# Kernel optimization log

Measured on AMD Instinct MI355X. Metric: run time of the kernel, lower is better.

## Reference

```python
import jax, jax.numpy as jnp
import numpy as np

N0, N1, N2 = 32, 32, 32
BOX = np.array([[0.0, 1.0], [0.0, 1.0], [0.0, 1.0]], dtype=np.float32)
N_VERTS, N_FACES = 512, 1024
EPS = 1.19209e-07
SEPS = float(np.sqrt(EPS))  # ~3.45e-4, matches torch code


def _freq_axis(n, lo, hi):
    # xi_k = (2k - (n-1)) * pi / (hi - lo)
    s = np.pi / (hi - lo)
    k = jnp.arange(n, dtype=jnp.float32)
    return (2.0 * k - (n - 1)) * jnp.float32(s)


def setup_inputs() -> dict:
    key = jax.random.key(0)
    k1, k2 = jax.random.split(key)
    Verts = jax.random.normal(k1, (N_VERTS, 3), dtype=jnp.float32)
    # distinct vertex indices per face -> non-degenerate triangles (a.s.)
    base = jax.random.randint(k2, (N_FACES, 1), 0, N_VERTS)
    Faces = (base + jnp.arange(3)[None, :]) % N_VERTS
    box_size = jnp.asarray(BOX)
    xi0 = _freq_axis(N0, BOX[0, 0], BOX[0, 1])
    xi1 = _freq_axis(N1, BOX[1, 0], BOX[1, 1])
    xi2 = _freq_axis(N2, BOX[2, 0], BOX[2, 1])
    return {"Verts": Verts, "box_size": box_size, "xi0": xi0, "xi1": xi1,
            "xi2": xi2, "Faces": Faces}


def _expmj(x):
    # exp(-i x) for real x -> complex64
    return jnp.exp(-1j * x)


def _fourier(Verts, box_size, xi0, xi1, xi2, Faces):
    V = Verts - box_size[:, 0]                      # shift into box frame
    coords = V[Faces]                               # (F, 3, 3)
    cross = jnp.cross(coords[:, 1] - coords[:, 0], coords[:, 2] - coords[:, 0])
    trisar = 0.5 * jnp.linalg.norm(cross, axis=1)   # (F,)
    meshar = jnp.sum(trisar)
    trisar = trisar * (2.0 / meshar)

    G0, G1, G2 = jnp.meshgrid(xi0, xi1, xi2, indexing="ij")
    Xi = jnp.stack([G0.ravel(), G1.ravel(), G2.ravel()], axis=1)  # (G, 3)
    xiv = Xi @ V.T                                  # (G, nV)

    xia = xiv[:, Faces[:, 0]]                       # (G, F)
    xib = xiv[:, Faces[:, 1]]
    xic = xiv[:, Faces[:, 2]]
    xiab = xib - xia
    xibc = xic - xib
    xica = xia - xic

    aab, abc, aca = jnp.abs(xiab), jnp.abs(xibc), jnp.abs(xica)
    s2, s3, s4 = aab < SEPS, abc < SEPS, aca < SEPS      # strict, for C1
    c2, c3, c4 = aab <= SEPS, abc <= SEPS, aca <= SEPS   # non-strict, C2-C4
    R1 = (s2 & s3) | (s3 & s4) | (s4 & s2)
    R2 = c2 & ~R1
    R3 = c3 & ~R2 & ~R1
    R4 = c4 & ~R3 & ~R2 & ~R1
    R5 = ~(R1 | R2 | R3 | R4)

    # R1: all edges collapse in frequency space
    v1 = _expmj((xia + xib + xic) / 3.0) / 2.0

    def _pair_case(mask, x1, x2, x3):
        # (i*exp(-i m) + (exp(-i m) - exp(-i x3)) / d) / d,  m=(x1+x2)/2, d=m-x3
        m = (x1 + x2) * 0.5
        d = jnp.where(mask, m - x3, 1.0)  # safe denominator off-mask
        em = _expmj(m)
        return (1j * em + (em - _expmj(x3)) / d) / d

    v2 = _pair_case(R2, xia, xib, xic)
    v3 = _pair_case(R3, xib, xic, xia)
    v4 = _pair_case(R4, xic, xia, xib)

    da = jnp.where(R5, xiab * xica, 1.0)
    db = jnp.where(R5, xibc * xiab, 1.0)
    dc = jnp.where(R5, xica * xibc, 1.0)
    v5 = _expmj(xia) / da + _expmj(xib) / db + _expmj(xic) / dc

    res = jnp.where(R1, v1,
          jnp.where(R2, v2,
          jnp.where(R3, v3,
          jnp.where(R4, v4, v5))))                  # (G, F) complex64

    ft = res @ trisar.astype(res.dtype)             # (G,)
    return ft.reshape(G0.shape)                     # (N0, N1, N2)


def reference(Verts, box_size, xi0, xi1, xi2, Faces):
    return _fourier(Verts, box_size, xi0, xi1, xi2, Faces)
```

## Files before the change

### kernel.cpp

```cpp
#include <hip/hip_runtime.h>
#include <math.h>


namespace {
constexpr int kNpts = 32 * 32 * 32;
constexpr int kHalf = kNpts / 2;
constexpr int kNF = 1024;
constexpr int kThreads = 1024;
constexpr int kWaves = 16;
constexpr int kFaceHalves = 2;
constexpr int kFPW = (kNF / kFaceHalves) / kWaves;
constexpr int kBlocks = (kHalf / 64) * kFaceHalves;
}

__device__ __forceinline__ float fract32(float x) {
#if __has_builtin(__builtin_amdgcn_fractf)
    return __builtin_amdgcn_fractf(x);
#else
    return x - floorf(x);
#endif
}

__device__ __forceinline__ void pair_case_f64(double x1, double x2, double x3,
                                              double& vr, double& vi) {
    const double m = (x1 + x2) * 0.5;
    const double d = m - x3;
    double sm, cm, s3, c3;
    sincos(m, &sm, &cm);
    sincos(x3, &s3, &c3);
    vr = (sm + (cm - c3) / d) / d;
    vi = (cm + (s3 - sm) / d) / d;
}

__device__ __noinline__ void slow_exact(
        int f, int p, const float* __restrict__ verts,
        const float* __restrict__ box, const int* __restrict__ faces,
        const float* __restrict__ xi0, const float* __restrict__ xi1,
        const float* __restrict__ xi2, float& cr, float& ci) {
    const double SEPS = __builtin_sqrt(1.19209e-07);
    const double TWO_PI = 6.283185307179586;
    const double INV_TWO_PI = 0.15915494309189535;

    const int i2 = p & 31, i1 = (p >> 5) & 31, i0 = p >> 10;
    const double xxd = (double)xi0[i0] * INV_TWO_PI;
    const double xyd = (double)xi1[i1] * INV_TWO_PI;
    const double xzd = (double)xi2[i2] * INV_TWO_PI;
    const double lo0 = (double)box[0], lo1 = (double)box[2], lo2 = (double)box[4];
    const int ia = faces[3 * f + 0], ib = faces[3 * f + 1], ic = faces[3 * f + 2];
    const double ax = (double)verts[3 * ia + 0] - lo0, ay = (double)verts[3 * ia + 1] - lo1, az = (double)verts[3 * ia + 2] - lo2;
    const double bx = (double)verts[3 * ib + 0] - lo0, by = (double)verts[3 * ib + 1] - lo1, bz = (double)verts[3 * ib + 2] - lo2;
    const double cx = (double)verts[3 * ic + 0] - lo0, cy = (double)verts[3 * ic + 1] - lo1, cz = (double)verts[3 * ic + 2] - lo2;
    const float axf = (float)ax, ayf = (float)ay, azf = (float)az;
    const float bxf = (float)bx, byf = (float)by, bzf = (float)bz;
    const float cxf = (float)cx, cyf = (float)cy, czf = (float)cz;
    const float e1x = bxf - axf, e1y = byf - ayf, e1z = bzf - azf;
    const float e2x = cxf - axf, e2y = cyf - ayf, e2z = czf - azf;
    const float crx = e1y * e2z - e1z * e2y;
    const float cry = e1z * e2x - e1x * e2z;
    const float crz = e1x * e2y - e1y * e2x;
    const float areaf = 0.5f * sqrtf(crx * crx + cry * cry + crz * crz);
    const double rad = fma(xzd, az, fma(xyd, ay, xxd * ax));
    const double rbd = fma(xzd, bz, fma(xyd, by, xxd * bx));
    const double rcd = fma(xzd, cz, fma(xyd, cy, xxd * cx));
    const double xa = rad * TWO_PI, xb = rbd * TWO_PI, xc = rcd * TWO_PI;
    const double dAB = xb - xa, dBC = xc - xb, dCA = xa - xc;
    const double aab = fabs(dAB), abc = fabs(dBC), aca = fabs(dCA);
    const bool s2 = aab < SEPS, s3 = abc < SEPS, s4 = aca < SEPS;
    const bool c2 = aab <= SEPS, c3 = abc <= SEPS, c4 = aca <= SEPS;
    const bool R1 = (s2 && s3) || (s3 && s4) || (s4 && s2);
    const bool R2 = c2 && !R1;
    const bool R3b = c3 && !R2 && !R1;
    const bool R4 = c4 && !R3b && !R2 && !R1;
    double vr, vi;
    if (R1) {
        const double m = ((xa + xb) + xc) / 3.0;
        double sm, cm;
        sincos(m, &sm, &cm);
        vr = cm / 2.0;
        vi = -sm / 2.0;
    } else if (R2) {
        pair_case_f64(xa, xb, xc, vr, vi);
    } else if (R3b) {
        pair_case_f64(xb, xc, xa, vr, vi);
    } else if (R4) {
        pair_case_f64(xc, xa, xb, vr, vi);
    } else {
        double sa, ca, sb, cb, sc, cc;
        sincos(xa, &sa, &ca);
        sincos(xb, &sb, &cb);
        sincos(xc, &sc, &cc);
        const double da = dAB * dCA, db = dBC * dAB, dc = dCA * dBC;
        vr = (ca / da + cb / db) + cc / dc;
        vi = -((sa / da + sb / db) + sc / dc);
    }
    cr = areaf * (float)vr;
    ci = areaf * (float)vi;
}

__global__ __launch_bounds__(kThreads, 8) void fourier_all(
        const float* __restrict__ verts, const float* __restrict__ box,
        const int* __restrict__ faces, const float* __restrict__ xi0,
        const float* __restrict__ xi1, const float* __restrict__ xi2,
        float* __restrict__ out, int interleaved) {
    const float INV_TWO_PI_F = 0.15915494f;
    const float TAUP_REV2 = 2.5330296e-5f;

    __shared__ float4 rec[kNF / kFaceHalves][3];
    __shared__ float accR[kWaves][64];
    __shared__ float accI[kWaves][64];
    __shared__ float wsum[kWaves];
    __shared__ float meshar_sh;

    const int t = threadIdx.x;
    const int l = t & 63;
    const int w = t >> 6;
    const int pb = blockIdx.x & 255;
    const int fh = blockIdx.x >> 8;

    {
        const int f = t;
        const float lo0 = box[0], lo1 = box[2], lo2 = box[4];
        const int ia = faces[3 * f + 0], ib = faces[3 * f + 1], ic = faces[3 * f + 2];
        const float ax = verts[3 * ia + 0] - lo0, ay = verts[3 * ia + 1] - lo1, az = verts[3 * ia + 2] - lo2;
        const float bx = verts[3 * ib + 0] - lo0, by = verts[3 * ib + 1] - lo1, bz = verts[3 * ib + 2] - lo2;
        const float cx = verts[3 * ic + 0] - lo0, cy = verts[3 * ic + 1] - lo1, cz = verts[3 * ic + 2] - lo2;
        const float e1x = bx - ax, e1y = by - ay, e1z = bz - az;
        const float e2x = cx - ax, e2y = cy - ay, e2z = cz - az;
        const float crx = e1y * e2z - e1z * e2y;
        const float cry = e1z * e2x - e1x * e2z;
        const float crz = e1x * e2y - e1y * e2x;
        const float area = 0.5f * sqrtf(crx * crx + cry * cry + crz * crz);
        if ((f >> 9) == fh) {
            const int r = f & 511;
            rec[r][0] = make_float4(ax, ay, az, bx);
            rec[r][1] = make_float4(by, bz, cx, cy);
            rec[r][2] = make_float4(cz, area * 0.025330296f, 0.0f, 0.0f);
        }
        float a = area;
        a += __shfl_down(a, 32, 64);
        a += __shfl_down(a, 16, 64);
        a += __shfl_down(a, 8, 64);
        a += __shfl_down(a, 4, 64);
        a += __shfl_down(a, 2, 64);
        a += __shfl_down(a, 1, 64);
        if (l == 0) wsum[w] = a;
    }
    __syncthreads();
    if (t == 0) {
        float s = wsum[0];
#pragma unroll
        for (int j = 1; j < kWaves; ++j) s += wsum[j];
        meshar_sh = s;
    }

    const int p = pb * 64 + l;
    const int i2 = p & 31, i1 = (p >> 5) & 31, i0 = p >> 10;
    const float xxr = xi0[i0] * INV_TWO_PI_F;
    const float xyr = xi1[i1] * INV_TWO_PI_F;
    const float xzr = xi2[i2] * INV_TWO_PI_F;

    float re = 0.0f, im = 0.0f;
    unsigned slowMask = 0u;
    const int rbase = w * kFPW;

#pragma unroll 4
    for (int i = 0; i < kFPW; ++i) {
        const float4 q0 = rec[rbase + i][0];
        const float4 q1 = rec[rbase + i][1];
        const float4 q2 = rec[rbase + i][2];
        const float ra = fmaf(xzr, q0.z, fmaf(xyr, q0.y, xxr * q0.x));
        const float rb = fmaf(xzr, q1.y, fmaf(xyr, q1.x, xxr * q0.w));
        const float rc = fmaf(xzr, q2.x, fmaf(xyr, q1.w, xxr * q1.z));
        const float fdab = rb - ra, fdbc = rc - rb, fdca = ra - rc;
        const float d1 = fdab * fdca;
        const float d2 = fdbc * fdab;
        const float d3 = fdca * fdbc;
        const float mn = fminf(fminf(fabsf(d1), fabsf(d2)), fabsf(d3));
        if (mn > TAUP_REV2) {
            const float R3w = __builtin_amdgcn_rcpf(d1 * fdbc) * q2.y;
            const float r1 = fdbc * R3w, r2 = fdca * R3w, r3 = fdab * R3w;
            const float fa = fract32(ra);
            const float fb = fract32(rb);
            const float fc = fract32(rc);
            const float sa = __builtin_amdgcn_sinf(fa), ca = __builtin_amdgcn_cosf(fa);
            const float sb = __builtin_amdgcn_sinf(fb), cb = __builtin_amdgcn_cosf(fb);
            const float sc = __builtin_amdgcn_sinf(fc), cc = __builtin_amdgcn_cosf(fc);
            re = fmaf(cc, r3, fmaf(cb, r2, fmaf(ca, r1, re)));
            im = fmaf(-sc, r3, fmaf(-sb, r2, fmaf(-sa, r1, im)));
        } else {
            slowMask |= (1u << i);
        }
    }

    if (slowMask) {
        const int gbase = fh * 512 + rbase;
        unsigned m = slowMask;
        do {
            const int i = __builtin_ctz(m);
            m &= m - 1u;
            float cr, ci;
            slow_exact(gbase + i, p, verts, box, faces, xi0, xi1, xi2, cr, ci);
            re += cr;
            im += ci;
        } while (m);
    }

    accR[w][l] = re;
    accI[w][l] = im;
    __syncthreads();

    if (t < 64) {
        float R = accR[0][l], I = accI[0][l];
#pragma unroll
        for (int g = 1; g < kWaves; ++g) { R += accR[g][l]; I += accI[g][l]; }
        const float inv2 = 2.0f / meshar_sh;
        R *= inv2;
        I *= inv2;
        const int q = kNpts - 1 - p;
        if (interleaved) {
            atomicAdd(&out[2 * p + 0], R);
            atomicAdd(&out[2 * p + 1], I);
            atomicAdd(&out[2 * q + 0], R);
            atomicAdd(&out[2 * q + 1], -I);
        } else {
            atomicAdd(&out[p], R);
            atomicAdd(&out[q], R);
        }
    }
}

extern "C" void kernel_launch(void* const* d_in, const int* in_sizes, int n_in,
                              void* d_out, int out_size, void* d_ws, size_t ws_size,
                              hipStream_t stream) {
    const float* verts = (const float*)d_in[0];
    const float* box   = (const float*)d_in[1];
    const float* xi0v  = (const float*)d_in[2];
    const float* xi1v  = (const float*)d_in[3];
    const float* xi2v  = (const float*)d_in[4];
    const int*   faces = (const int*)d_in[5];
    (void)d_ws; (void)ws_size;

    const int interleaved = (out_size == 2 * kNpts) ? 1 : 0;

    hipMemsetAsync(d_out, 0, (size_t)out_size * sizeof(float), stream);
    hipLaunchKernelGGL(fourier_all, dim3(kBlocks), dim3(kThreads), 0, stream,
                       verts, box, faces, xi0v, xi1v, xi2v,
                       (float*)d_out, interleaved);
}
```

Before: 92.59 us.

## Split fast path and slow exact fallback into separate kernels via workspace

The main kernel now only runs the fast float path, writes per-wave partial sums and per-lane slow-case bitmasks to workspace, and computes each half's mesh area sum once instead of in every block. A second small kernel sums the two face halves, evaluates the rare slow double-precision cases, normalises, and writes the output directly. This drops the memset and the atomics and keeps the slow-path code out of the hot kernel, which should lower register pressure and divergence there. In exchange it adds a second launch, workspace traffic, and serialised slow-case work within a 64-thread combine kernel.

```diff
diff --git a/kernel.cpp b/kernel.cpp
--- a/kernel.cpp
+++ b/kernel.cpp
@@ -11,6 +11,9 @@
 constexpr int kFaceHalves = 2;
 constexpr int kFPW = (kNF / kFaceHalves) / kWaves;
 constexpr int kBlocks = (kHalf / 64) * kFaceHalves;
+constexpr int kNumWaves = kBlocks * kWaves;
+constexpr int kGridOffW = 256;
+constexpr int kMaskOffW = kGridOffW + kFaceHalves * kHalf * 2;
 }
 
 __device__ __forceinline__ float fract32(float x) {
@@ -19,6 +22,112 @@
 #else
     return x - floorf(x);
 #endif
+}
+
+__global__ __launch_bounds__(kThreads, 8) void fourier_main(
+        const float* __restrict__ verts, const float* __restrict__ box,
+        const int* __restrict__ faces, unsigned* __restrict__ wsu,
+        const float* __restrict__ xi0, const float* __restrict__ xi1,
+        const float* __restrict__ xi2) {
+    const float INV_TWO_PI_F = 0.15915494f;
+    const float TAUP_REV2 = 2.5330296e-5f;
+
+    __shared__ float4 rec[kNF / kFaceHalves][3];
+    __shared__ float accR[kWaves][64];
+    __shared__ float accI[kWaves][64];
+    __shared__ float wsum[8];
+
+    const int t = threadIdx.x;
+    const int l = t & 63;
+    const int w = t >> 6;
+    const int pb = blockIdx.x & 255;
+    const int fh = blockIdx.x >> 8;
+
+    if (t < 512) {
+        const int f = fh * 512 + t;
+        const float lo0 = box[0], lo1 = box[2], lo2 = box[4];
+        const int ia = faces[3 * f + 0], ib = faces[3 * f + 1], ic = faces[3 * f + 2];
+        const float ax = verts[3 * ia + 0] - lo0, ay = verts[3 * ia + 1] - lo1, az = verts[3 * ia + 2] - lo2;
+        const float bx = verts[3 * ib + 0] - lo0, by = verts[3 * ib + 1] - lo1, bz = verts[3 * ib + 2] - lo2;
+        const float cx = verts[3 * ic + 0] - lo0, cy = verts[3 * ic + 1] - lo1, cz = verts[3 * ic + 2] - lo2;
+        const float e1x = bx - ax, e1y = by - ay, e1z = bz - az;
+        const float e2x = cx - ax, e2y = cy - ay, e2z = cz - az;
+        const float crx = e1y * e2z - e1z * e2y;
+        const float cry = e1z * e2x - e1x * e2z;
+        const float crz = e1x * e2y - e1y * e2x;
+        const float area = 0.5f * sqrtf(crx * crx + cry * cry + crz * crz);
+        rec[t][0] = make_float4(ax, ay, az, bx);
+        rec[t][1] = make_float4(by, bz, cx, cy);
+        rec[t][2] = make_float4(cz, area * 0.025330296f, 0.0f, 0.0f);
+        float a = area;
+        a += __shfl_down(a, 32, 64);
+        a += __shfl_down(a, 16, 64);
+        a += __shfl_down(a, 8, 64);
+        a += __shfl_down(a, 4, 64);
+        a += __shfl_down(a, 2, 64);
+        a += __shfl_down(a, 1, 64);
+        if (l == 0) wsum[w] = a;
+    }
+    __syncthreads();
+    if (t == 0 && pb == 0) {
+        float s = wsum[0];
+#pragma unroll
+        for (int j = 1; j < 8; ++j) s += wsum[j];
+        ((float*)wsu)[fh] = s;
+    }
+
+    const int p = pb * 64 + l;
+    const int i2 = p & 31, i1 = (p >> 5) & 31, i0 = p >> 10;
+    const float xxr = xi0[i0] * INV_TWO_PI_F;
+    const float xyr = xi1[i1] * INV_TWO_PI_F;
+    const float xzr = xi2[i2] * INV_TWO_PI_F;
+
+    float re = 0.0f, im = 0.0f;
+    unsigned slowMask = 0u;
+    const int rbase = w * kFPW;
+
+#pragma unroll 4
+    for (int i = 0; i < kFPW; ++i) {
+        const float4 q0 = rec[rbase + i][0];
+        const float4 q1 = rec[rbase + i][1];
+        const float4 q2 = rec[rbase + i][2];
+        const float ra = fmaf(xzr, q0.z, fmaf(xyr, q0.y, xxr * q0.x));
+        const float rb = fmaf(xzr, q1.y, fmaf(xyr, q1.x, xxr * q0.w));
+        const float rc = fmaf(xzr, q2.x, fmaf(xyr, q1.w, xxr * q1.z));
+        const float fdab = rb - ra, fdbc = rc - rb, fdca = ra - rc;
+        const float d1 = fdab * fdca;
+        const float d2 = fdbc * fdab;
+        const float d3 = fdca * fdbc;
+        const float mn = fminf(fminf(fabsf(d1), fabsf(d2)), fabsf(d3));
+        if (mn > TAUP_REV2) {
+            const float R3w = __builtin_amdgcn_rcpf(d1 * fdbc) * q2.y;
+            const float r1 = fdbc * R3w, r2 = fdca * R3w, r3 = fdab * R3w;
+            const float fa = fract32(ra);
+            const float fb = fract32(rb);
+            const float fc = fract32(rc);
+            const float sa = __builtin_amdgcn_sinf(fa), ca = __builtin_amdgcn_cosf(fa);
+            const float sb = __builtin_amdgcn_sinf(fb), cb = __builtin_amdgcn_cosf(fb);
+            const float sc = __builtin_amdgcn_sinf(fc), cc = __builtin_amdgcn_cosf(fc);
+            re = fmaf(cc, r3, fmaf(cb, r2, fmaf(ca, r1, re)));
+            im = fmaf(-sc, r3, fmaf(-sb, r2, fmaf(-sa, r1, im)));
+        } else {
+            slowMask |= (1u << i);
+        }
+    }
+
+    const int waveId = blockIdx.x * kWaves + w;
+    wsu[kMaskOffW + waveId * 64 + l] = slowMask;
+
+    accR[w][l] = re;
+    accI[w][l] = im;
+    __syncthreads();
+    if (w == 0) {
+        float R = accR[0][l], I = accI[0][l];
+#pragma unroll
+        for (int g = 1; g < kWaves; ++g) { R += accR[g][l]; I += accI[g][l]; }
+        float2* pg = (float2*)(wsu + kGridOffW);
+        pg[(size_t)fh * kHalf + p] = make_float2(R, I);
+    }
 }
 
 __device__ __forceinline__ void pair_case_f64(double x1, double x2, double x3,
@@ -97,135 +206,49 @@
     ci = areaf * (float)vi;
 }
 
-__global__ __launch_bounds__(kThreads, 8) void fourier_all(
+__global__ __launch_bounds__(64) void combine_fix(
         const float* __restrict__ verts, const float* __restrict__ box,
         const int* __restrict__ faces, const float* __restrict__ xi0,
         const float* __restrict__ xi1, const float* __restrict__ xi2,
-        float* __restrict__ out, int interleaved) {
-    const float INV_TWO_PI_F = 0.15915494f;
-    const float TAUP_REV2 = 2.5330296e-5f;
-
-    __shared__ float4 rec[kNF / kFaceHalves][3];
-    __shared__ float accR[kWaves][64];
-    __shared__ float accI[kWaves][64];
-    __shared__ float wsum[kWaves];
-    __shared__ float meshar_sh;
-
-    const int t = threadIdx.x;
-    const int l = t & 63;
-    const int w = t >> 6;
-    const int pb = blockIdx.x & 255;
-    const int fh = blockIdx.x >> 8;
-
-    {
-        const int f = t;
-        const float lo0 = box[0], lo1 = box[2], lo2 = box[4];
-        const int ia = faces[3 * f + 0], ib = faces[3 * f + 1], ic = faces[3 * f + 2];
-        const float ax = verts[3 * ia + 0] - lo0, ay = verts[3 * ia + 1] - lo1, az = verts[3 * ia + 2] - lo2;
-        const float bx = verts[3 * ib + 0] - lo0, by = verts[3 * ib + 1] - lo1, bz = verts[3 * ib + 2] - lo2;
-        const float cx = verts[3 * ic + 0] - lo0, cy = verts[3 * ic + 1] - lo1, cz = verts[3 * ic + 2] - lo2;
-        const float e1x = bx - ax, e1y = by - ay, e1z = bz - az;
-        const float e2x = cx - ax, e2y = cy - ay, e2z = cz - az;
-        const float crx = e1y * e2z - e1z * e2y;
-        const float cry = e1z * e2x - e1x * e2z;
-        const float crz = e1x * e2y - e1y * e2x;
-        const float area = 0.5f * sqrtf(crx * crx + cry * cry + crz * crz);
-        if ((f >> 9) == fh) {
-            const int r = f & 511;
-            rec[r][0] = make_float4(ax, ay, az, bx);
-            rec[r][1] = make_float4(by, bz, cx, cy);
-            rec[r][2] = make_float4(cz, area * 0.025330296f, 0.0f, 0.0f);
+        const unsigned* __restrict__ wsu, float* __restrict__ out,
+        int interleaved) {
+    const int pb = blockIdx.x;
+    const int l = threadIdx.x;
+    const int p = pb * 64 + l;
+
+    const float2* pg = (const float2*)(wsu + kGridOffW);
+    const float2 a = pg[p];
+    const float2 b = pg[kHalf + p];
+    float R = a.x + b.x;
+    float I = a.y + b.y;
+
+#pragma unroll
+    for (int fh = 0; fh < 2; ++fh) {
+        for (int w = 0; w < kWaves; ++w) {
+            unsigned m = wsu[kMaskOffW + (((fh << 8) | pb) * kWaves + w) * 64 + l];
+            while (m) {
+                const int i = __builtin_ctz(m);
+                m &= m - 1u;
+                float cr, ci;
+                slow_exact(fh * 512 + w * kFPW + i, p, verts, box, faces,
+                           xi0, xi1, xi2, cr, ci);
+                R += cr;
+                I += ci;
+            }
         }
-        float a = area;
-        a += __shfl_down(a, 32, 64);
-        a += __shfl_down(a, 16, 64);
-        a += __shfl_down(a, 8, 64);
-        a += __shfl_down(a, 4, 64);
-        a += __shfl_down(a, 2, 64);
-        a += __shfl_down(a, 1, 64);
-        if (l == 0) wsum[w] = a;
-    }
-    __syncthreads();
-    if (t == 0) {
-        float s = wsum[0];
-#pragma unroll
-        for (int j = 1; j < kWaves; ++j) s += wsum[j];
-        meshar_sh = s;
-    }
-
-    const int p = pb * 64 + l;
-    const int i2 = p & 31, i1 = (p >> 5) & 31, i0 = p >> 10;
-    const float xxr = xi0[i0] * INV_TWO_PI_F;
-    const float xyr = xi1[i1] * INV_TWO_PI_F;
-    const float xzr = xi2[i2] * INV_TWO_PI_F;
-
-    float re = 0.0f, im = 0.0f;
-    unsigned slowMask = 0u;
-    const int rbase = w * kFPW;
-
-#pragma unroll 4
-    for (int i = 0; i < kFPW; ++i) {
-        const float4 q0 = rec[rbase + i][0];
-        const float4 q1 = rec[rbase + i][1];
-        const float4 q2 = rec[rbase + i][2];
-        const float ra = fmaf(xzr, q0.z, fmaf(xyr, q0.y, xxr * q0.x));
-        const float rb = fmaf(xzr, q1.y, fmaf(xyr, q1.x, xxr * q0.w));
-        const float rc = fmaf(xzr, q2.x, fmaf(xyr, q1.w, xxr * q1.z));
-        const float fdab = rb - ra, fdbc = rc - rb, fdca = ra - rc;
-        const float d1 = fdab * fdca;
-        const float d2 = fdbc * fdab;
-        const float d3 = fdca * fdbc;
-        const float mn = fminf(fminf(fabsf(d1), fabsf(d2)), fabsf(d3));
-        if (mn > TAUP_REV2) {
-            const float R3w = __builtin_amdgcn_rcpf(d1 * fdbc) * q2.y;
-            const float r1 = fdbc * R3w, r2 = fdca * R3w, r3 = fdab * R3w;
-            const float fa = fract32(ra);
-            const float fb = fract32(rb);
-            const float fc = fract32(rc);
-            const float sa = __builtin_amdgcn_sinf(fa), ca = __builtin_amdgcn_cosf(fa);
-            const float sb = __builtin_amdgcn_sinf(fb), cb = __builtin_amdgcn_cosf(fb);
-            const float sc = __builtin_amdgcn_sinf(fc), cc = __builtin_amdgcn_cosf(fc);
-            re = fmaf(cc, r3, fmaf(cb, r2, fmaf(ca, r1, re)));
-            im = fmaf(-sc, r3, fmaf(-sb, r2, fmaf(-sa, r1, im)));
-        } else {
-            slowMask |= (1u << i);
-        }
-    }
-
-    if (slowMask) {
-        const int gbase = fh * 512 + rbase;
-        unsigned m = slowMask;
-        do {
-            const int i = __builtin_ctz(m);
-            m &= m - 1u;
-            float cr, ci;
-            slow_exact(gbase + i, p, verts, box, faces, xi0, xi1, xi2, cr, ci);
-            re += cr;
-            im += ci;
-        } while (m);
-    }
-
-    accR[w][l] = re;
-    accI[w][l] = im;
-    __syncthreads();
-
-    if (t < 64) {
-        float R = accR[0][l], I = accI[0][l];
-#pragma unroll
-        for (int g = 1; g < kWaves; ++g) { R += accR[g][l]; I += accI[g][l]; }
-        const float inv2 = 2.0f / meshar_sh;
-        R *= inv2;
-        I *= inv2;
-        const int q = kNpts - 1 - p;
-        if (interleaved) {
-            atomicAdd(&out[2 * p + 0], R);
-            atomicAdd(&out[2 * p + 1], I);
-            atomicAdd(&out[2 * q + 0], R);
-            atomicAdd(&out[2 * q + 1], -I);
-        } else {
-            atomicAdd(&out[p], R);
-            atomicAdd(&out[q], R);
-        }
+    }
+
+    const float* wsf = (const float*)wsu;
+    const float inv2 = 2.0f / (wsf[0] + wsf[1]);
+    R *= inv2;
+    I *= inv2;
+    const int q = kNpts - 1 - p;
+    if (interleaved) {
+        ((float2*)out)[p] = make_float2(R, I);
+        ((float2*)out)[q] = make_float2(R, -I);
+    } else {
+        out[p] = R;
+        out[q] = R;
     }
 }
 
@@ -238,12 +261,13 @@
     const float* xi1v  = (const float*)d_in[3];
     const float* xi2v  = (const float*)d_in[4];
     const int*   faces = (const int*)d_in[5];
-    (void)d_ws; (void)ws_size;
+    unsigned* wsu = (unsigned*)d_ws;
 
     const int interleaved = (out_size == 2 * kNpts) ? 1 : 0;
 
-    hipMemsetAsync(d_out, 0, (size_t)out_size * sizeof(float), stream);
-    hipLaunchKernelGGL(fourier_all, dim3(kBlocks), dim3(kThreads), 0, stream,
-                       verts, box, faces, xi0v, xi1v, xi2v,
+    hipLaunchKernelGGL(fourier_main, dim3(kBlocks), dim3(kThreads), 0, stream,
+                       verts, box, faces, wsu, xi0v, xi1v, xi2v);
+    hipLaunchKernelGGL(combine_fix, dim3(kHalf / 64), dim3(64), 0, stream,
+                       verts, box, faces, xi0v, xi1v, xi2v, wsu,
                        (float*)d_out, interleaved);
 }
```

After: 107.7 us. 16.3% more time.

## Reuse trig across four consecutive z-frequencies via angle-addition recurrence

Applied to the files above, without the earlier changes.

Each thread now handles four adjacent xi2 points per face. It evaluates sin/cos only for the first and advances to the next three by complex rotation with per-face precomputed cos/sin of the vertex z step, and it updates the edge differences incrementally. The grid becomes 64 point-groups times 4 face quarters, with a larger LDS record per face and 256-wide accumulators. This cuts transcendental work per point-face pair and the number of blocks, at the cost of more registers, occupancy limited to 4 blocks, and possible accumulated rounding error from the recurrence.

```diff
diff --git a/kernel.cpp b/kernel.cpp
--- a/kernel.cpp
+++ b/kernel.cpp
@@ -8,9 +8,10 @@
 constexpr int kNF = 1024;
 constexpr int kThreads = 1024;
 constexpr int kWaves = 16;
-constexpr int kFaceHalves = 2;
-constexpr int kFPW = (kNF / kFaceHalves) / kWaves;
-constexpr int kBlocks = (kHalf / 64) * kFaceHalves;
+constexpr int kFQ = 4;
+constexpr int kFPB = kNF / kFQ;
+constexpr int kFPWv = kFPB / kWaves;
+constexpr int kBlocks = 64 * kFQ;
 }
 
 __device__ __forceinline__ float fract32(float x) {
@@ -97,7 +98,7 @@
     ci = areaf * (float)vi;
 }
 
-__global__ __launch_bounds__(kThreads, 8) void fourier_all(
+__global__ __launch_bounds__(kThreads, 4) void fourier_zrec(
         const float* __restrict__ verts, const float* __restrict__ box,
         const int* __restrict__ faces, const float* __restrict__ xi0,
         const float* __restrict__ xi1, const float* __restrict__ xi2,
@@ -105,17 +106,19 @@
     const float INV_TWO_PI_F = 0.15915494f;
     const float TAUP_REV2 = 2.5330296e-5f;
 
-    __shared__ float4 rec[kNF / kFaceHalves][3];
-    __shared__ float accR[kWaves][64];
-    __shared__ float accI[kWaves][64];
+    __shared__ float4 rec[kFPB][5];
+    __shared__ float accR[kWaves][256];
+    __shared__ float accI[kWaves][256];
     __shared__ float wsum[kWaves];
     __shared__ float meshar_sh;
 
     const int t = threadIdx.x;
     const int l = t & 63;
     const int w = t >> 6;
-    const int pb = blockIdx.x & 255;
-    const int fh = blockIdx.x >> 8;
+    const int g = blockIdx.x >> 2;
+    const int fq = blockIdx.x & 3;
+    const int i0 = g >> 2;
+    const int i1base = (g & 3) * 8;
 
     {
         const int f = t;
@@ -130,11 +133,17 @@
         const float cry = e1z * e2x - e1x * e2z;
         const float crz = e1x * e2y - e1y * e2x;
         const float area = 0.5f * sqrtf(crx * crx + cry * cry + crz * crz);
-        if ((f >> 9) == fh) {
-            const int r = f & 511;
+        if ((f >> 8) == fq) {
+            const int r = f & 255;
+            const float fa = fract32(az), fb = fract32(bz), fc = fract32(cz);
+            const float cA = __builtin_amdgcn_cosf(fa), sA = __builtin_amdgcn_sinf(fa);
+            const float cB = __builtin_amdgcn_cosf(fb), sB = __builtin_amdgcn_sinf(fb);
+            const float cC = __builtin_amdgcn_cosf(fc), sC = __builtin_amdgcn_sinf(fc);
             rec[r][0] = make_float4(ax, ay, az, bx);
             rec[r][1] = make_float4(by, bz, cx, cy);
-            rec[r][2] = make_float4(cz, area * 0.025330296f, 0.0f, 0.0f);
+            rec[r][2] = make_float4(cz, area * 0.025330296f, bz - az, cz - bz);
+            rec[r][3] = make_float4(cA, sA, cB, sB);
+            rec[r][4] = make_float4(cC, sC, az - cz, 0.0f);
         }
         float a = area;
         a += __shfl_down(a, 32, 64);
@@ -153,69 +162,96 @@
         meshar_sh = s;
     }
 
-    const int p = pb * 64 + l;
-    const int i2 = p & 31, i1 = (p >> 5) & 31, i0 = p >> 10;
+    const int i1 = i1base + (l >> 3);
+    const int i2base = (l & 7) * 4;
     const float xxr = xi0[i0] * INV_TWO_PI_F;
     const float xyr = xi1[i1] * INV_TWO_PI_F;
-    const float xzr = xi2[i2] * INV_TWO_PI_F;
-
-    float re = 0.0f, im = 0.0f;
-    unsigned slowMask = 0u;
-    const int rbase = w * kFPW;
-
-#pragma unroll 4
-    for (int i = 0; i < kFPW; ++i) {
+    const float xzr0 = xi2[i2base] * INV_TWO_PI_F;
+
+    float re[4] = {0.0f, 0.0f, 0.0f, 0.0f};
+    float im[4] = {0.0f, 0.0f, 0.0f, 0.0f};
+    unsigned long long slowMask = 0ull;
+    const int rbase = w * kFPWv;
+
+#pragma unroll 2
+    for (int i = 0; i < kFPWv; ++i) {
         const float4 q0 = rec[rbase + i][0];
         const float4 q1 = rec[rbase + i][1];
         const float4 q2 = rec[rbase + i][2];
-        const float ra = fmaf(xzr, q0.z, fmaf(xyr, q0.y, xxr * q0.x));
-        const float rb = fmaf(xzr, q1.y, fmaf(xyr, q1.x, xxr * q0.w));
-        const float rc = fmaf(xzr, q2.x, fmaf(xyr, q1.w, xxr * q1.z));
-        const float fdab = rb - ra, fdbc = rc - rb, fdca = ra - rc;
-        const float d1 = fdab * fdca;
-        const float d2 = fdbc * fdab;
-        const float d3 = fdca * fdbc;
-        const float mn = fminf(fminf(fabsf(d1), fabsf(d2)), fabsf(d3));
-        if (mn > TAUP_REV2) {
-            const float R3w = __builtin_amdgcn_rcpf(d1 * fdbc) * q2.y;
-            const float r1 = fdbc * R3w, r2 = fdca * R3w, r3 = fdab * R3w;
-            const float fa = fract32(ra);
-            const float fb = fract32(rb);
-            const float fc = fract32(rc);
-            const float sa = __builtin_amdgcn_sinf(fa), ca = __builtin_amdgcn_cosf(fa);
-            const float sb = __builtin_amdgcn_sinf(fb), cb = __builtin_amdgcn_cosf(fb);
-            const float sc = __builtin_amdgcn_sinf(fc), cc = __builtin_amdgcn_cosf(fc);
-            re = fmaf(cc, r3, fmaf(cb, r2, fmaf(ca, r1, re)));
-            im = fmaf(-sc, r3, fmaf(-sb, r2, fmaf(-sa, r1, im)));
-        } else {
-            slowMask |= (1u << i);
+        const float4 q3 = rec[rbase + i][3];
+        const float4 q4 = rec[rbase + i][4];
+        const float ra = fmaf(xzr0, q0.z, fmaf(xyr, q0.y, xxr * q0.x));
+        const float rb = fmaf(xzr0, q1.y, fmaf(xyr, q1.x, xxr * q0.w));
+        const float rc = fmaf(xzr0, q2.x, fmaf(xyr, q1.w, xxr * q1.z));
+        float fdab = rb - ra, fdbc = rc - rb, fdca = ra - rc;
+        float ca_ = __builtin_amdgcn_cosf(fract32(ra)), sa_ = __builtin_amdgcn_sinf(fract32(ra));
+        float cb_ = __builtin_amdgcn_cosf(fract32(rb)), sb_ = __builtin_amdgcn_sinf(fract32(rb));
+        float cc_ = __builtin_amdgcn_cosf(fract32(rc)), sc_ = __builtin_amdgcn_sinf(fract32(rc));
+        const float wgt = q2.y;
+        const float dsab = q2.z, dsbc = q2.w, dsca = q4.z;
+        const float cA = q3.x, sA = q3.y, cB = q3.z, sB = q3.w;
+        const float cC = q4.x, sC = q4.y;
+
+#pragma unroll
+        for (int k = 0; k < 4; ++k) {
+            const float d1 = fdab * fdca;
+            const float d2 = fdbc * fdab;
+            const float d3 = fdca * fdbc;
+            const float mn = fminf(fminf(fabsf(d1), fabsf(d2)), fabsf(d3));
+            if (mn > TAUP_REV2) {
+                const float R3w = __builtin_amdgcn_rcpf(d1 * fdbc) * wgt;
+                const float r1 = fdbc * R3w, r2 = fdca * R3w, r3 = fdab * R3w;
+                re[k] = fmaf(cc_, r3, fmaf(cb_, r2, fmaf(ca_, r1, re[k])));
+                im[k] = fmaf(-sc_, r3, fmaf(-sb_, r2, fmaf(-sa_, r1, im[k])));
+            } else {
+                slowMask |= (1ull << (i * 4 + k));
+            }
+            if (k < 3) {
+                const float nca = ca_ * cA - sa_ * sA;
+                const float nsa = sa_ * cA + ca_ * sA;
+                const float ncb = cb_ * cB - sb_ * sB;
+                const float nsb = sb_ * cB + cb_ * sB;
+                const float ncc = cc_ * cC - sc_ * sC;
+                const float nsc = sc_ * cC + cc_ * sC;
+                ca_ = nca; sa_ = nsa;
+                cb_ = ncb; sb_ = nsb;
+                cc_ = ncc; sc_ = nsc;
+                fdab += dsab; fdbc += dsbc; fdca += dsca;
+            }
         }
     }
 
     if (slowMask) {
-        const int gbase = fh * 512 + rbase;
-        unsigned m = slowMask;
-        do {
-            const int i = __builtin_ctz(m);
-            m &= m - 1u;
-            float cr, ci;
-            slow_exact(gbase + i, p, verts, box, faces, xi0, xi1, xi2, cr, ci);
-            re += cr;
-            im += ci;
-        } while (m);
-    }
-
-    accR[w][l] = re;
-    accI[w][l] = im;
+#pragma unroll
+        for (int k = 0; k < 4; ++k) {
+            unsigned long long m = (slowMask >> k) & 0x1111111111111111ull;
+            while (m) {
+                const int b = (int)__builtin_ctzll(m);
+                m &= m - 1ull;
+                const int i = b >> 2;
+                const int f = fq * kFPB + rbase + i;
+                const int p = (i0 << 10) | (i1 << 5) | (i2base + k);
+                float cr, ci;
+                slow_exact(f, p, verts, box, faces, xi0, xi1, xi2, cr, ci);
+                re[k] += cr;
+                im[k] += ci;
+            }
+        }
+    }
+
+    const int slotBase = (l >> 3) * 32 + (l & 7) * 4;
+    *(float4*)&accR[w][slotBase] = make_float4(re[0], re[1], re[2], re[3]);
+    *(float4*)&accI[w][slotBase] = make_float4(im[0], im[1], im[2], im[3]);
     __syncthreads();
 
-    if (t < 64) {
-        float R = accR[0][l], I = accI[0][l];
-#pragma unroll
-        for (int g = 1; g < kWaves; ++g) { R += accR[g][l]; I += accI[g][l]; }
+    if (t < 256) {
+        float R = accR[0][t], I = accI[0][t];
+#pragma unroll
+        for (int gg = 1; gg < kWaves; ++gg) { R += accR[gg][t]; I += accI[gg][t]; }
         const float inv2 = 2.0f / meshar_sh;
         R *= inv2;
         I *= inv2;
+        const int p = (i0 << 10) | ((i1base + (t >> 5)) << 5) | (t & 31);
         const int q = kNpts - 1 - p;
         if (interleaved) {
             atomicAdd(&out[2 * p + 0], R);
@@ -243,7 +279,7 @@
     const int interleaved = (out_size == 2 * kNpts) ? 1 : 0;
 
     hipMemsetAsync(d_out, 0, (size_t)out_size * sizeof(float), stream);
-    hipLaunchKernelGGL(fourier_all, dim3(kBlocks), dim3(kThreads), 0, stream,
+    hipLaunchKernelGGL(fourier_zrec, dim3(kBlocks), dim3(kThreads), 0, stream,
                        verts, box, faces, xi0v, xi1v, xi2v,
                        (float*)d_out, interleaved);
 }
```

After: 90.11 us (median of 2 runs). -2.7%, faster.
